# Performance work log

Hardware: AMD Instinct MI355X
Metric: run time of the kernel (lower is better)

## Reference

```python
import jax, jax.numpy as jnp
import numpy as np

N_NODES, D_NODE = 100000, 128
N_EDGES, D_EDGE = 1000000, 32
D_IN = 2 * D_NODE + D_EDGE  # 288
H1, H2, D_OUT = 128, 64, 1


def setup_inputs() -> dict:
    key = jax.random.key(0)
    ks = jax.random.split(key, 9)
    x = jax.random.normal(ks[0], (N_NODES, D_NODE), dtype=jnp.float32)
    edge_index = jax.random.randint(ks[1], (2, N_EDGES), 0, N_NODES, dtype=jnp.int64)
    edge_features = jax.random.normal(ks[2], (N_EDGES, D_EDGE), dtype=jnp.float32)
    def lin(kw, kb, fan_in, fan_out):
        bound = 1.0 / np.sqrt(fan_in)
        W = jax.random.uniform(kw, (fan_in, fan_out), minval=-bound, maxval=bound, dtype=jnp.float32)
        b = jax.random.uniform(kb, (fan_out,), minval=-bound, maxval=bound, dtype=jnp.float32)
        return W, b
    W1, b1 = lin(ks[3], ks[4], D_IN, H1)
    W2, b2 = lin(ks[5], ks[6], H1, H2)
    W3, b3 = lin(ks[7], ks[8], H2, D_OUT)
    return {"x": x, "edge_index": edge_index, "edge_features": edge_features,
            "W1": W1, "b1": b1, "W2": W2, "b2": b2, "W3": W3, "b3": b3}


def reference(x, edge_index, edge_features, W1, b1, W2, b2, W3, b3):
    origin, destination = edge_index[0], edge_index[1]
    # [E, 2*D_NODE + D_EDGE]
    z = jnp.concatenate([x[origin], x[destination], edge_features], axis=1)
    z = jax.nn.leaky_relu(z @ W1 + b1)  # negative_slope=0.01, matches torch default
    z = jax.nn.leaky_relu(z @ W2 + b2)
    z = z @ W3 + b3
    return z.reshape(-1)
```

## Files before the change

kernel.cpp:

```cpp
#include <hip/hip_runtime.h>

#define N_NODES 100000
#define N_EDGES 1000000

typedef __attribute__((ext_vector_type(8))) short bf16x8;
typedef __attribute__((ext_vector_type(4))) float f32x4;
typedef __attribute__((ext_vector_type(4))) unsigned u32x4;

static __device__ __forceinline__ short f2bf(float f) {
    unsigned u = __float_as_uint(f);
    u = (u + 0x7fffu + ((u >> 16) & 1u)) >> 16;
    return (short)u;
}
static __device__ __forceinline__ float bf2f(unsigned short s) {
    return __uint_as_float(((unsigned)s) << 16);
}
static __device__ __forceinline__ float lrelu(float x) {
    return fmaxf(x, 0.01f * x);
}
static __device__ __forceinline__ unsigned cvtpk(float lo, float hi) {
    unsigned r;
    asm("v_cvt_pk_bf16_f32 %0, %1, %2" : "=v"(r) : "v"(lo), "v"(hi));
    return r;
}

__global__ __launch_bounds__(256) void precompute_mfma(
    const float* __restrict__ x, const float* __restrict__ W1,
    const float* __restrict__ b1, unsigned short* __restrict__ Pb,
    unsigned short* __restrict__ Qb)
{
    const int t    = threadIdx.x;
    const int lane = t & 63;
    const int w    = t >> 6;
    const int q    = lane >> 4;
    const int n15  = lane & 15;
    const int chb  = 64 * w;

    bf16x8 afrag[4][4];
    #pragma unroll
    for (int mtl = 0; mtl < 4; ++mtl) {
        const int ch = chb + 16 * mtl + n15;
        const float* wcol = (ch < 128) ? (W1 + ch) : (W1 + 128 * 128 + (ch - 128));
        #pragma unroll
        for (int ks = 0; ks < 4; ++ks)
            #pragma unroll
            for (int j = 0; j < 8; ++j)
                afrag[mtl][ks][j] = f2bf(wcol[(size_t)(32 * ks + 8 * q + j) * 128]);
    }
    float b1r[16];
    #pragma unroll
    for (int mtl = 0; mtl < 4; ++mtl)
        #pragma unroll
        for (int r = 0; r < 4; ++r) {
            const int ch = chb + 16 * mtl + 4 * q + r;
            b1r[mtl * 4 + r] = (ch < 128) ? b1[ch] : 0.0f;
        }

    unsigned short* tbase = (w < 2) ? Pb : Qb;
    const int mtb = 4 * (w & 1);

    for (int tile = blockIdx.x; tile < N_NODES / 16; tile += gridDim.x) {
        const int n0 = tile * 16;
        const float* xrow = x + (size_t)(n0 + n15) * 128;

        bf16x8 bfr[4];
        #pragma unroll
        for (int ks = 0; ks < 4; ++ks) {
            f32x4 xa = *(const f32x4*)(xrow + 32 * ks + 8 * q);
            f32x4 xb = *(const f32x4*)(xrow + 32 * ks + 8 * q + 4);
            u32x4 bu;
            bu[0] = cvtpk(xa[0], xa[1]);
            bu[1] = cvtpk(xa[2], xa[3]);
            bu[2] = cvtpk(xb[0], xb[1]);
            bu[3] = cvtpk(xb[2], xb[3]);
            bfr[ks] = __builtin_bit_cast(bf16x8, bu);
        }
        #pragma unroll
        for (int mtl = 0; mtl < 4; ++mtl) {
            f32x4 acc = {0.f, 0.f, 0.f, 0.f};
            #pragma unroll
            for (int ks = 0; ks < 4; ++ks)
                acc = __builtin_amdgcn_mfma_f32_16x16x32_bf16(afrag[mtl][ks], bfr[ks], acc, 0, 0, 0);
            unsigned* dst = (unsigned*)(tbase + (size_t)(n0 + n15) * 128 + q * 32 + (mtb + mtl) * 4);
            dst[0] = cvtpk(acc[0] + b1r[mtl * 4 + 0], acc[1] + b1r[mtl * 4 + 1]);
            dst[1] = cvtpk(acc[2] + b1r[mtl * 4 + 2], acc[3] + b1r[mtl * 4 + 3]);
        }
    }
}

__global__ __launch_bounds__(256, 3) void edge_mfma(
    const int* __restrict__ ei, const float* __restrict__ ef,
    const float* __restrict__ W1, const float* __restrict__ W2,
    const float* __restrict__ b2, const float* __restrict__ W3,
    const float* __restrict__ b3, const unsigned short* __restrict__ Pb,
    const unsigned short* __restrict__ Qb, float* __restrict__ out)
{
    __shared__ unsigned short hbuf[4][16 * 136 + 8];
    __shared__ unsigned short w2s[16 * 64 * 8];
    const int t    = threadIdx.x;
    const int lane = t & 63;
    const int w    = t >> 6;
    const int q    = lane >> 4;
    const int n15  = lane & 15;
    unsigned short* hb = &hbuf[w][0];

    bf16x8 a1[8];
    #pragma unroll
    for (int mt = 0; mt < 8; ++mt)
        #pragma unroll
        for (int j = 0; j < 8; ++j)
            a1[mt][j] = f2bf(W1[(size_t)(256 + 8 * q + j) * 128 + 16 * mt + n15]);

    {
        const int mt2 = w;
        #pragma unroll
        for (int ks = 0; ks < 4; ++ks) {
            bf16x8 f;
            #pragma unroll
            for (int j = 0; j < 8; ++j)
                f[j] = f2bf(W2[(size_t)(32 * ks + 8 * q + j) * 64 + 16 * mt2 + n15]);
            *(bf16x8*)&w2s[(((mt2 << 2) | ks) * 64 + lane) * 8] = f;
        }
    }

    unsigned b2w3[16];
    #pragma unroll
    for (int mt2 = 0; mt2 < 4; ++mt2)
        #pragma unroll
        for (int r = 0; r < 4; ++r) {
            const int ch = 16 * mt2 + 4 * q + r;
            b2w3[mt2 * 4 + r] = (unsigned)(unsigned short)f2bf(b2[ch])
                              | ((unsigned)(unsigned short)f2bf(W3[ch]) << 16);
        }
    const float b3v = b3[0];

    __syncthreads();

    const int nTiles  = N_EDGES / 16;
    const int wid     = blockIdx.x * 4 + w;
    const int wstride = gridDim.x * 4;
    if (wid >= nTiles) return;

    int tile0 = wid;
    int tile1 = tile0 + wstride;
    bool have1 = tile1 < nTiles;

    int oi0, di0; f32x4 ea0, eb0;
    {
        const int e0 = tile0 * 16;
        oi0 = ei[e0 + n15];
        di0 = ei[N_EDGES + e0 + n15];
        ea0 = *(const f32x4*)(ef + (size_t)(e0 + n15) * 32 + 8 * q);
        eb0 = *(const f32x4*)(ef + (size_t)(e0 + n15) * 32 + 8 * q + 4);
    }
    int oi1 = 0, di1 = 0; f32x4 ea1 = ea0, eb1 = eb0;
    if (have1) {
        const int e1 = tile1 * 16;
        oi1 = ei[e1 + n15];
        di1 = ei[N_EDGES + e1 + n15];
        ea1 = *(const f32x4*)(ef + (size_t)(e1 + n15) * 32 + 8 * q);
        eb1 = *(const f32x4*)(ef + (size_t)(e1 + n15) * 32 + 8 * q + 4);
    }
    bf16x8 pvb[4], qvb[4];
    {
        const unsigned short* prow = Pb + (size_t)oi0 * 128 + q * 32;
        const unsigned short* qrow = Qb + (size_t)di0 * 128 + q * 32;
        #pragma unroll
        for (int c = 0; c < 4; ++c) {
            pvb[c] = *(const bf16x8*)(prow + 8 * c);
            qvb[c] = *(const bf16x8*)(qrow + 8 * c);
        }
    }

    while (true) {
        u32x4 befu;
        befu[0] = cvtpk(ea0[0], ea0[1]);
        befu[1] = cvtpk(ea0[2], ea0[3]);
        befu[2] = cvtpk(eb0[0], eb0[1]);
        befu[3] = cvtpk(eb0[2], eb0[3]);
        const bf16x8 bef = __builtin_bit_cast(bf16x8, befu);

        const int  tile2 = tile1 + wstride;
        const bool have2 = have1 && (tile2 < nTiles);
        int oi2 = oi1, di2 = di1; f32x4 ea2 = ea1, eb2 = eb1;
        if (have2) {
            const int e2 = tile2 * 16;
            oi2 = ei[e2 + n15];
            di2 = ei[N_EDGES + e2 + n15];
            ea2 = *(const f32x4*)(ef + (size_t)(e2 + n15) * 32 + 8 * q);
            eb2 = *(const f32x4*)(ef + (size_t)(e2 + n15) * 32 + 8 * q + 4);
        }

        #pragma unroll
        for (int mt = 0; mt < 8; ++mt) {
            f32x4 z = {0.f, 0.f, 0.f, 0.f};
            f32x4 h = __builtin_amdgcn_mfma_f32_16x16x32_bf16(a1[mt], bef, z, 0, 0, 0);
            const int c = mt >> 1, off = (mt & 1) * 4;
            float v0 = lrelu(h[0] + bf2f((unsigned short)pvb[c][off + 0]) + bf2f((unsigned short)qvb[c][off + 0]));
            float v1 = lrelu(h[1] + bf2f((unsigned short)pvb[c][off + 1]) + bf2f((unsigned short)qvb[c][off + 1]));
            float v2 = lrelu(h[2] + bf2f((unsigned short)pvb[c][off + 2]) + bf2f((unsigned short)qvb[c][off + 2]));
            float v3 = lrelu(h[3] + bf2f((unsigned short)pvb[c][off + 3]) + bf2f((unsigned short)qvb[c][off + 3]));
            unsigned* d = (unsigned*)&hb[n15 * 136 + 16 * mt + 4 * q];
            d[0] = cvtpk(v0, v1);
            d[1] = cvtpk(v2, v3);
        }

        if (have1) {
            const unsigned short* prow = Pb + (size_t)oi1 * 128 + q * 32;
            const unsigned short* qrow = Qb + (size_t)di1 * 128 + q * 32;
            #pragma unroll
            for (int c = 0; c < 4; ++c) {
                pvb[c] = *(const bf16x8*)(prow + 8 * c);
                qvb[c] = *(const bf16x8*)(qrow + 8 * c);
            }
        }

        __asm__ __volatile__("s_waitcnt lgkmcnt(0)" ::: "memory");

        f32x4 acc2[4] = {{0.f,0.f,0.f,0.f},{0.f,0.f,0.f,0.f},{0.f,0.f,0.f,0.f},{0.f,0.f,0.f,0.f}};
        #pragma unroll
        for (int ks = 0; ks < 4; ++ks) {
            const bf16x8 hfrag = *(const bf16x8*)&hb[n15 * 136 + 32 * ks + 8 * q];
            #pragma unroll
            for (int mt2 = 0; mt2 < 4; ++mt2) {
                const bf16x8 a2f = *(const bf16x8*)&w2s[(((mt2 << 2) | ks) * 64 + lane) * 8];
                acc2[mt2] = __builtin_amdgcn_mfma_f32_16x16x32_bf16(a2f, hfrag, acc2[mt2], 0, 0, 0);
            }
        }

        float s = 0.0f;
        #pragma unroll
        for (int mt2 = 0; mt2 < 4; ++mt2)
            #pragma unroll
            for (int r = 0; r < 4; ++r) {
                const unsigned u = b2w3[mt2 * 4 + r];
                float v = acc2[mt2][r] + bf2f((unsigned short)(u & 0xffffu));
                v = lrelu(v);
                s += v * __uint_as_float(u & 0xffff0000u);
            }
        s += __shfl_xor(s, 16);
        s += __shfl_xor(s, 32);
        if (q == 0) out[tile0 * 16 + n15] = s + b3v;

        if (!have1) break;
        tile0 = tile1; tile1 = tile2; have1 = have2;
        oi1 = oi2; di1 = di2;
        ea0 = ea1; eb0 = eb1; ea1 = ea2; eb1 = eb2;
    }
}

extern "C" void kernel_launch(void* const* d_in, const int* in_sizes, int n_in,
                              void* d_out, int out_size, void* d_ws, size_t ws_size,
                              hipStream_t stream) {
    const float* x   = (const float*)d_in[0];
    const int*   ei  = (const int*)d_in[1];
    const float* ef  = (const float*)d_in[2];
    const float* W1  = (const float*)d_in[3];
    const float* b1  = (const float*)d_in[4];
    const float* W2  = (const float*)d_in[5];
    const float* b2  = (const float*)d_in[6];
    const float* W3  = (const float*)d_in[7];
    const float* b3  = (const float*)d_in[8];
    float*       out = (float*)d_out;

    unsigned short* Pb = (unsigned short*)d_ws;
    unsigned short* Qb = Pb + (size_t)N_NODES * 128;

    precompute_mfma<<<2048, 256, 0, stream>>>(x, W1, b1, Pb, Qb);
    edge_mfma<<<1024, 256, 0, stream>>>(ei, ef, W1, W2, b2, W3, b3, Pb, Qb, out);
}
```

Before: 354.8 us.

## Keep layer-1 activations in registers by permuting W2 K-order; move W1 slice to LDS

The layer-2 MFMA B-fragment is now built directly from the layer-1 MFMA output registers. To make that possible, the K (channel) order of the W2 fragments stored in shared memory is permuted to match the accumulator layout, which removes the per-tile LDS write, the lgkmcnt wait and the LDS read of the hidden buffer. The edge-feature slice of W1 now lives in shared memory instead of 8 register fragments. This frees VGPRs but adds LDS reads in the inner loop. The grid also shrinks from 1024 to 768 blocks.

```diff
diff --git a/kernel.cpp b/kernel.cpp
--- a/kernel.cpp
+++ b/kernel.cpp
@@ -95,21 +95,23 @@
     const float* __restrict__ b3, const unsigned short* __restrict__ Pb,
     const unsigned short* __restrict__ Qb, float* __restrict__ out)
 {
-    __shared__ unsigned short hbuf[4][16 * 136 + 8];
     __shared__ unsigned short w2s[16 * 64 * 8];
+    __shared__ unsigned short a1s[8 * 64 * 8];
     const int t    = threadIdx.x;
     const int lane = t & 63;
     const int w    = t >> 6;
     const int q    = lane >> 4;
     const int n15  = lane & 15;
-    unsigned short* hb = &hbuf[w][0];
-
-    bf16x8 a1[8];
-    #pragma unroll
-    for (int mt = 0; mt < 8; ++mt)
+
+    #pragma unroll
+    for (int i = 0; i < 2; ++i) {
+        const int mt = 2 * w + i;
+        bf16x8 f;
         #pragma unroll
         for (int j = 0; j < 8; ++j)
-            a1[mt][j] = f2bf(W1[(size_t)(256 + 8 * q + j) * 128 + 16 * mt + n15]);
+            f[j] = f2bf(W1[(size_t)(256 + 8 * q + j) * 128 + 16 * mt + n15]);
+        *(bf16x8*)&a1s[(mt * 64 + lane) * 8] = f;
+    }
 
     {
         const int mt2 = w;
@@ -117,8 +119,10 @@
         for (int ks = 0; ks < 4; ++ks) {
             bf16x8 f;
             #pragma unroll
-            for (int j = 0; j < 8; ++j)
-                f[j] = f2bf(W2[(size_t)(32 * ks + 8 * q + j) * 64 + 16 * mt2 + n15]);
+            for (int j = 0; j < 8; ++j) {
+                const int ch = 32 * ks + ((j < 4) ? (4 * q + j) : (16 + 4 * q + (j - 4)));
+                f[j] = f2bf(W2[(size_t)ch * 64 + 16 * mt2 + n15]);
+            }
             *(bf16x8*)&w2s[(((mt2 << 2) | ks) * 64 + lane) * 8] = f;
         }
     }
@@ -186,23 +190,25 @@
         if (have2) {
             const int e2 = tile2 * 16;
             oi2 = ei[e2 + n15];
+            ndi2:
             di2 = ei[N_EDGES + e2 + n15];
             ea2 = *(const f32x4*)(ef + (size_t)(e2 + n15) * 32 + 8 * q);
             eb2 = *(const f32x4*)(ef + (size_t)(e2 + n15) * 32 + 8 * q + 4);
         }
 
+        u32x4 hfu[4];
         #pragma unroll
         for (int mt = 0; mt < 8; ++mt) {
+            const bf16x8 a1f = *(const bf16x8*)&a1s[(mt * 64 + lane) * 8];
             f32x4 z = {0.f, 0.f, 0.f, 0.f};
-            f32x4 h = __builtin_amdgcn_mfma_f32_16x16x32_bf16(a1[mt], bef, z, 0, 0, 0);
+            f32x4 h = __builtin_amdgcn_mfma_f32_16x16x32_bf16(a1f, bef, z, 0, 0, 0);
             const int c = mt >> 1, off = (mt & 1) * 4;
             float v0 = lrelu(h[0] + bf2f((unsigned short)pvb[c][off + 0]) + bf2f((unsigned short)qvb[c][off + 0]));
             float v1 = lrelu(h[1] + bf2f((unsigned short)pvb[c][off + 1]) + bf2f((unsigned short)qvb[c][off + 1]));
             float v2 = lrelu(h[2] + bf2f((unsigned short)pvb[c][off + 2]) + bf2f((unsigned short)qvb[c][off + 2]));
             float v3 = lrelu(h[3] + bf2f((unsigned short)pvb[c][off + 3]) + bf2f((unsigned short)qvb[c][off + 3]));
-            unsigned* d = (unsigned*)&hb[n15 * 136 + 16 * mt + 4 * q];
-            d[0] = cvtpk(v0, v1);
-            d[1] = cvtpk(v2, v3);
+            hfu[mt >> 1][(mt & 1) * 2 + 0] = cvtpk(v0, v1);
+            hfu[mt >> 1][(mt & 1) * 2 + 1] = cvtpk(v2, v3);
         }
 
         if (have1) {
@@ -215,12 +221,10 @@
             }
         }
 
-        __asm__ __volatile__("s_waitcnt lgkmcnt(0)" ::: "memory");
-
         f32x4 acc2[4] = {{0.f,0.f,0.f,0.f},{0.f,0.f,0.f,0.f},{0.f,0.f,0.f,0.f},{0.f,0.f,0.f,0.f}};
         #pragma unroll
         for (int ks = 0; ks < 4; ++ks) {
-            const bf16x8 hfrag = *(const bf16x8*)&hb[n15 * 136 + 32 * ks + 8 * q];
+            const bf16x8 hfrag = __builtin_bit_cast(bf16x8, hfu[ks]);
             #pragma unroll
             for (int mt2 = 0; mt2 < 4; ++mt2) {
                 const bf16x8 a2f = *(const bf16x8*)&w2s[(((mt2 << 2) | ks) * 64 + lane) * 8];
@@ -267,5 +271,5 @@
     unsigned short* Qb = Pb + (size_t)N_NODES * 128;
 
     precompute_mfma<<<2048, 256, 0, stream>>>(x, W1, b1, Pb, Qb);
-    edge_mfma<<<1024, 256, 0, stream>>>(ei, ef, W1, W2, b2, W3, b3, Pb, Qb, out);
-}
+    edge_mfma<<<768, 256, 0, stream>>>(ei, ef, W1, W2, b2, W3, b3, Pb, Qb, out);
+}
```

After: 351.5 us. Within noise of the previous version (-0.9%).
